# Kernel optimization log

Hardware: AMD Instinct MI355X
Metric: run time of the kernel (lower is better)

Reference implementation:

```python
import jax, jax.numpy as jnp
from jax import lax
import numpy as np

B, T, F_IN, H = 64, 128, 12, 128  # batch, seq_len, input/output features, hidden


def _uinit(key, shape, fan):
    return jax.random.uniform(key, shape, jnp.float32, -1.0, 1.0) / np.float32(np.sqrt(fan))


def setup_inputs() -> dict:
    key = jax.random.key(0)
    ks = jax.random.split(key, 12)
    inp = {
        "x": jax.random.normal(ks[0], (B, T, F_IN), jnp.float32),
        # encoder LSTM (gate order i,f,g,o; b = b_ih + b_hh folded together)
        "enc_Wih": _uinit(ks[1], (4 * H, F_IN), H),
        "enc_Whh": _uinit(ks[2], (4 * H, H), H),
        "enc_b": _uinit(ks[3], (4 * H,), H),
        # decoder LSTM (input is the 12-dim teacher-forced x slice)
        "dec_Wih": _uinit(ks[4], (4 * H, F_IN), H),
        "dec_Whh": _uinit(ks[5], (4 * H, H), H),
        "dec_b": _uinit(ks[6], (4 * H,), H),
        # attention: Linear(2H -> H) with bias, then v: Linear(H -> 1, no bias)
        "attn_W": _uinit(ks[7], (H, 2 * H), 2 * H),
        "attn_b": _uinit(ks[8], (H,), 2 * H),
        "v_w": _uinit(ks[9], (H,), H),
        # output layer: Linear(2H -> F_IN)  (intended width; see notes)
        "out_W": _uinit(ks[10], (F_IN, 2 * H), 2 * H),
        "out_b": _uinit(ks[11], (F_IN,), 2 * H),
    }
    return inp


def _lstm_cell(xt, h, c, Wih, Whh, b):
    z = xt @ Wih.T + h @ Whh.T + b  # [B, 4H]
    i, f, g, o = jnp.split(z, 4, axis=-1)
    c = jax.nn.sigmoid(f) * c + jax.nn.sigmoid(i) * jnp.tanh(g)
    h = jax.nn.sigmoid(o) * jnp.tanh(c)
    return h, c


def reference(x, enc_Wih, enc_Whh, enc_b, dec_Wih, dec_Whh, dec_b,
              attn_W, attn_b, v_w, out_W, out_b):
    b_, t_, _ = x.shape
    hdim = enc_Whh.shape[1]
    xs = jnp.swapaxes(x, 0, 1)  # [T, B, F]
    h0 = jnp.zeros((b_, hdim), x.dtype)
    c0 = jnp.zeros((b_, hdim), x.dtype)

    def enc_step(carry, xt):
        h, c = carry
        h, c = _lstm_cell(xt, h, c, enc_Wih, enc_Whh, enc_b)
        return (h, c), h

    (hT, cT), enc_hs = lax.scan(enc_step, (h0, c0), xs)
    enc_out = jnp.swapaxes(enc_hs, 0, 1)  # [B, T, H]

    # split attn weight: cat(hidden, enc_out) @ W.T == hidden@W1.T + enc_out@W2.T
    W1, W2 = attn_W[:, :hdim], attn_W[:, hdim:]
    enc_proj = jnp.einsum("bth,gh->btg", enc_out, W2)  # precompute encoder side

    def dec_step(carry, xt):
        h, c = carry
        h, c = _lstm_cell(xt, h, c, dec_Wih, dec_Whh, dec_b)
        energy = jnp.tanh((h @ W1.T)[:, None, :] + enc_proj + attn_b)  # [B,T,H]
        score = jnp.einsum("bth,h->bt", energy, v_w)
        w = jax.nn.softmax(score, axis=1)  # attention over encoder time
        ctx = jnp.einsum("bt,bth->bh", w, enc_out)
        return (h, c), jnp.concatenate([h, ctx], axis=-1)  # [B, 2H]

    _, dec_ys = lax.scan(dec_step, (hT, cT), xs)
    dec_out = jnp.swapaxes(dec_ys, 0, 1)  # [B, T, 2H]
    return dec_out @ out_W.T + out_b  # [B, T, F]
```

## Files before the change

### kernel.cpp

```cpp
#include <hip/hip_runtime.h>
#include <hip/hip_bf16.h>

#define BB 64
#define TT 128
#define FIN 12
#define HH 128

#define LOG2E 1.4426950408889634f
#define TWO_LOG2E 2.8853900817779268f

typedef float f2v __attribute__((ext_vector_type(2)));
union F4 { float4 v; f2v h[2]; };

__device__ __forceinline__ float fexp2(float x) { return __builtin_amdgcn_exp2f(x); }
__device__ __forceinline__ float frcp(float x)  { return __builtin_amdgcn_rcpf(x); }

__device__ __forceinline__ float tanh_f(float x) {
  return 1.0f - 2.0f * frcp(1.0f + fexp2(TWO_LOG2E * x));
}
__device__ __forceinline__ float sigm_f(float x) {
  return frcp(1.0f + fexp2(-LOG2E * x));
}

template <int CTRL>
__device__ __forceinline__ float dpp_addstage(float v) {
  int s = __builtin_amdgcn_update_dpp(0, __float_as_int(v), CTRL, 0xF, 0xF, true);
  return v + __int_as_float(s);
}
__device__ __forceinline__ float red8(float v) {
  v = dpp_addstage<0xB1>(v);
  v = dpp_addstage<0x4E>(v);
  v = dpp_addstage<0x141>(v);
  return v;
}

#define PKFMA(acc, hh, ww) \
  asm("v_pk_fma_f32 %0, %1, %2, %0" : "+v"(acc) : "v"(hh), "v"(ww))

#define FMA4S(acc, s, v) do { \
  acc.x = fmaf((s), (v).x, acc.x); \
  acc.y = fmaf((s), (v).y, acc.y); \
  acc.z = fmaf((s), (v).z, acc.z); \
  acc.w = fmaf((s), (v).w, acc.w); } while (0)

#define ACC4(hv, wv, a) do { \
  a = fmaf((hv).x, (wv).x, a); a = fmaf((hv).y, (wv).y, a); \
  a = fmaf((hv).z, (wv).z, a); a = fmaf((hv).w, (wv).w, a); } while (0)

__device__ __forceinline__ void lstm_phase(
    const float* __restrict__ Wih, const float* __restrict__ Whh,
    const float* __restrict__ bias, float* __restrict__ Hout ,
    float* __restrict__ xs, float (*hbuf)[160], float* __restrict__ hist,
    const int tid, const int q, const int i, float& c)
{
  const int xo   = (q < 4) ? 3 * q : 0;
  const float xz = (q < 4) ? 1.0f : 0.0f;

  F4 wg[4][4];
  #pragma unroll
  for (int g = 0; g < 4; ++g)
    #pragma unroll
    for (int j = 0; j < 4; ++j)
      wg[g][j].v = *(const float4*)(Whh + ((g * HH + i) * HH) + 16 * q + 4 * j);

  float wx[4][3];
  #pragma unroll
  for (int g = 0; g < 4; ++g)
    #pragma unroll
    for (int j = 0; j < 3; ++j)
      wx[g][j] = Wih[(g * HH + i) * FIN + xo + j] * xz;

  const float bi = bias[i], bf = bias[HH + i], bg = bias[2 * HH + i], bo = bias[3 * HH + i];

  int ts = 0;
  #pragma unroll 1
  for (int half = 0; half < 2; ++half) {
    #pragma unroll 1
    for (int tt = 0; tt < 64; ++tt, ++ts) {
      const int t = half * 64 + tt;
      __syncthreads();
      const float* hb = (const float*)hbuf[ts & 1] + q * 20;
      F4 H[4];
      H[0].v = *(const float4*)(hb + 0);
      H[1].v = *(const float4*)(hb + 4);
      H[2].v = *(const float4*)(hb + 8);
      H[3].v = *(const float4*)(hb + 12);

      const float* xt = xs + t * FIN + xo;
      float x0 = xt[0], x1 = xt[1], x2 = xt[2];
      float ai = wx[0][0] * x0 + wx[0][1] * x1 + wx[0][2] * x2;
      float af = wx[1][0] * x0 + wx[1][1] * x1 + wx[1][2] * x2;
      float ag = wx[2][0] * x0 + wx[2][1] * x1 + wx[2][2] * x2;
      float ao = wx[3][0] * x0 + wx[3][1] * x1 + wx[3][2] * x2;

      f2v A0 = {0.f, 0.f}, A1 = {0.f, 0.f}, A2 = {0.f, 0.f}, A3 = {0.f, 0.f};
      #pragma unroll
      for (int j = 0; j < 4; ++j) {
        PKFMA(A0, H[j].h[0], wg[0][j].h[0]); PKFMA(A0, H[j].h[1], wg[0][j].h[1]);
        PKFMA(A1, H[j].h[0], wg[1][j].h[0]); PKFMA(A1, H[j].h[1], wg[1][j].h[1]);
        PKFMA(A2, H[j].h[0], wg[2][j].h[0]); PKFMA(A2, H[j].h[1], wg[2][j].h[1]);
        PKFMA(A3, H[j].h[0], wg[3][j].h[0]); PKFMA(A3, H[j].h[1], wg[3][j].h[1]);
      }
      ai += A0.x + A0.y; af += A1.x + A1.y;
      ag += A2.x + A2.y; ao += A3.x + A3.y;

      ai = red8(ai); af = red8(af); ag = red8(ag); ao = red8(ao);

      if (q == 0) {
        float zi = sigm_f(ai + bi);
        float zf = sigm_f(af + bf);
        float zg = tanh_f(ag + bg);
        float zo = sigm_f(ao + bo);
        c = fmaf(zf, c, zi * zg);
        float hn = zo * tanh_f(c);
        hbuf[(ts + 1) & 1][(i >> 4) * 20 + (i & 15)] = hn;
        hist[tt * HH + i] = hn;
      }
    }
    __syncthreads();
    {
      float4* dst = (float4*)(Hout + (size_t)(half * 64) * HH);
      const float4* src = (const float4*)hist;
      dst[tid]        = src[tid];
      dst[tid + 1024] = src[tid + 1024];
    }
  }
}

__global__ __launch_bounds__(1024, 4) void lstm_enc_kernel(
    const float* __restrict__ x,
    const float* __restrict__ eWih, const float* __restrict__ eWhh, const float* __restrict__ eb,
    float* __restrict__ encH, float* __restrict__ decH)
{
  const int b   = blockIdx.x;
  const int tid = threadIdx.x;
  const int q   = tid & 7;
  const int i   = tid >> 3;

  __shared__ __align__(16) float xs[TT * FIN];
  __shared__ __align__(16) float hbuf[2][160];
  __shared__ __align__(16) float hist[64 * HH];

  if (tid < (TT * FIN / 4))
    ((float4*)xs)[tid] = ((const float4*)(x + (size_t)b * TT * FIN))[tid];
  if (tid < 320) ((float*)hbuf)[tid] = 0.0f;
  float c = 0.0f;

  lstm_phase(eWih, eWhh, eb, encH + (size_t)b * TT * HH, xs, hbuf, hist, tid, q, i, c);

  if (q == 0) decH[(size_t)b * TT * HH + i] = c;
}

__global__ __launch_bounds__(1024, 4) void lstm_dec_p_kernel(
    const float* __restrict__ x,
    const float* __restrict__ dWih, const float* __restrict__ dWhh, const float* __restrict__ db,
    const float* __restrict__ attnW,
    const float* __restrict__ encH,
    float* __restrict__ decH, float* __restrict__ Pbuf)
{
  __shared__ __align__(16) float smem[12416];
  const int tid = threadIdx.x;

  if (blockIdx.x < 64) {
    const int b = blockIdx.x;
    const int q = tid & 7;
    const int i = tid >> 3;
    float* xs           = smem;
    float (*hbuf)[160]  = (float(*)[160])(smem + 1536);
    float* hist         = smem + 1856;

    if (tid < (TT * FIN / 4))
      ((float4*)xs)[tid] = ((const float4*)(x + (size_t)b * TT * FIN))[tid];
    if (tid < 128) {
      float hv = encH[((size_t)b * TT + 127) * HH + tid];
      hbuf[0][(tid >> 4) * 20 + (tid & 15)] = hv;
    }
    float c = 0.0f;
    if (q == 0) c = decH[(size_t)b * TT * HH + i];

    lstm_phase(dWih, dWhh, db, decH + (size_t)b * TT * HH, xs, hbuf, hist, tid, q, i, c);
  } else {
    const int pb = blockIdx.x - 64;
    const int b  = pb & 63;
    const int r0 = (pb >> 6) * 64;
    float* WT = smem;
    float* Xt = smem + 4224;

    const float* X = encH + ((size_t)b * TT + r0) * HH;
    ((float4*)Xt)[tid]        = ((const float4*)X)[tid];
    ((float4*)Xt)[tid + 1024] = ((const float4*)X)[tid + 1024];

    const float* W = attnW + HH;
    const int hq = tid & 31, rr = tid >> 5;
    const int h0 = 4 * hq;

    float4 acc0 = make_float4(0.f, 0.f, 0.f, 0.f);
    float4 acc1 = acc0;

    #pragma unroll 1
    for (int kb = 0; kb < 4; ++kb) {
      __syncthreads();
      {
        int h = tid >> 3, koff = (tid & 7) * 4;
        float4 v = *(const float4*)(W + h * 256 + kb * 32 + koff);
        WT[(koff + 0) * 132 + h] = v.x;
        WT[(koff + 1) * 132 + h] = v.y;
        WT[(koff + 2) * 132 + h] = v.z;
        WT[(koff + 3) * 132 + h] = v.w;
      }
      __syncthreads();
      const float* xr0 = Xt + (2 * rr) * 128 + kb * 32;
      const float* xr1 = xr0 + 128;
      #pragma unroll
      for (int k4 = 0; k4 < 32; k4 += 4) {
        float4 xa = *(const float4*)(xr0 + k4);
        float4 xb = *(const float4*)(xr1 + k4);
        float4 w0 = *(const float4*)&WT[(k4 + 0) * 132 + h0];
        float4 w1 = *(const float4*)&WT[(k4 + 1) * 132 + h0];
        float4 w2 = *(const float4*)&WT[(k4 + 2) * 132 + h0];
        float4 w3 = *(const float4*)&WT[(k4 + 3) * 132 + h0];
        FMA4S(acc0, xa.x, w0); FMA4S(acc0, xa.y, w1);
        FMA4S(acc0, xa.z, w2); FMA4S(acc0, xa.w, w3);
        FMA4S(acc1, xb.x, w0); FMA4S(acc1, xb.y, w1);
        FMA4S(acc1, xb.z, w2); FMA4S(acc1, xb.w, w3);
      }
    }
    acc0.x = fexp2(TWO_LOG2E * acc0.x); acc0.y = fexp2(TWO_LOG2E * acc0.y);
    acc0.z = fexp2(TWO_LOG2E * acc0.z); acc0.w = fexp2(TWO_LOG2E * acc0.w);
    acc1.x = fexp2(TWO_LOG2E * acc1.x); acc1.y = fexp2(TWO_LOG2E * acc1.y);
    acc1.z = fexp2(TWO_LOG2E * acc1.z); acc1.w = fexp2(TWO_LOG2E * acc1.w);
    float* O = Pbuf + ((size_t)b * TT + r0) * HH;
    *(float4*)(O + (2 * rr) * 128 + h0)     = acc0;
    *(float4*)(O + (2 * rr + 1) * 128 + h0) = acc1;
  }
}

__global__ __launch_bounds__(256, 2) void projA_kernel(
    const float* __restrict__ decH, const float* __restrict__ attnW,
    const float* __restrict__ attnb, float* __restrict__ Abuf)
{
  const int b  = blockIdx.x & 63;
  const int r0 = (blockIdx.x >> 6) * 16;
  const int tid = threadIdx.x;

  __shared__ __align__(16) float WT[64 * 128];
  __shared__ __align__(16) float Xt[16 * 128];

  const float* X = decH + ((size_t)b * TT + r0) * HH;
  const float* W = attnW;

  ((float4*)Xt)[tid]       = ((const float4*)X)[tid];
  ((float4*)Xt)[256 + tid] = ((const float4*)X)[256 + tid];

  const int hq = tid & 31, rr = tid >> 5;
  const int h0 = 4 * hq;

  float4 acc0 = *(const float4*)(attnb + h0);
  float4 acc1 = acc0;

  for (int kb = 0; kb < 2; ++kb) {
    __syncthreads();
    {
      int h = tid >> 1, koff = (tid & 1) * 32;
      #pragma unroll
      for (int j = 0; j < 8; ++j) {
        float4 v = *(const float4*)(W + h * 256 + kb * 64 + koff + 4 * j);
        int kp = koff + 4 * j;
        WT[(kp + 0) * 128 + h] = v.x;
        WT[(kp + 1) * 128 + h] = v.y;
        WT[(kp + 2) * 128 + h] = v.z;
        WT[(kp + 3) * 128 + h] = v.w;
      }
    }
    __syncthreads();
    const float* xr0 = Xt + (2 * rr) * 128 + kb * 64;
    const float* xr1 = xr0 + 128;
    #pragma unroll
    for (int k4 = 0; k4 < 64; k4 += 4) {
      float4 xa = *(const float4*)(xr0 + k4);
      float4 xb = *(const float4*)(xr1 + k4);
      float4 w0 = *(const float4*)&WT[(k4 + 0) * 128 + h0];
      float4 w1 = *(const float4*)&WT[(k4 + 1) * 128 + h0];
      float4 w2 = *(const float4*)&WT[(k4 + 2) * 128 + h0];
      float4 w3 = *(const float4*)&WT[(k4 + 3) * 128 + h0];
      FMA4S(acc0, xa.x, w0); FMA4S(acc0, xa.y, w1);
      FMA4S(acc0, xa.z, w2); FMA4S(acc0, xa.w, w3);
      FMA4S(acc1, xb.x, w0); FMA4S(acc1, xb.y, w1);
      FMA4S(acc1, xb.z, w2); FMA4S(acc1, xb.w, w3);
    }
  }
  acc0.x = fexp2(TWO_LOG2E * acc0.x); acc0.y = fexp2(TWO_LOG2E * acc0.y);
  acc0.z = fexp2(TWO_LOG2E * acc0.z); acc0.w = fexp2(TWO_LOG2E * acc0.w);
  acc1.x = fexp2(TWO_LOG2E * acc1.x); acc1.y = fexp2(TWO_LOG2E * acc1.y);
  acc1.z = fexp2(TWO_LOG2E * acc1.z); acc1.w = fexp2(TWO_LOG2E * acc1.w);
  float* O = Abuf + ((size_t)b * TT + r0) * HH;
  *(float4*)(O + (2 * rr) * 128 + h0)     = acc0;
  *(float4*)(O + (2 * rr + 1) * 128 + h0) = acc1;
}

#define AST 132

__global__ __launch_bounds__(512, 2) void attn_kernel(
    const float* __restrict__ encH, const float* __restrict__ decH,
    const float* __restrict__ Pbuf, const float* __restrict__ Abuf,
    const float* __restrict__ vw, const float* __restrict__ outW,
    const float* __restrict__ outb, float* __restrict__ out)
{
  const int b  = blockIdx.x >> 3;
  const int s0 = (blockIdx.x & 7) * 16;
  const int tid = threadIdx.x;

  __shared__ __align__(16) float buf[64 * 128];
  __shared__ __align__(16) float a_lds[16 * AST];
  __shared__ __align__(16) float sc[16 * AST];
  __shared__ __align__(16) float dh[16 * 128];
  __shared__ __align__(16) float vl[HH];

  ((float4*)dh)[tid] = ((const float4*)(decH + ((size_t)b * TT + s0) * HH))[tid];
  if (tid < 32) ((float4*)vl)[tid] = ((const float4*)vw)[tid];
  {
    int r = tid >> 5, c4 = (tid & 31) * 4;
    float4 av = *(const float4*)(Abuf + ((size_t)b * TT + s0 + r) * HH + c4);
    *(float4*)&a_lds[r * AST + c4] = av;
  }

  const int u  = tid & 31;
  const int sl = tid >> 5;
  const int uq = u & 15;
  const int uh = u >> 4;

  for (int half = 0; half < 2; ++half) {
    const int tbase = half * 64;
    __syncthreads();
    #pragma unroll
    for (int i = 0; i < 4; ++i) {
      int flat = i * 2048 + tid * 4;
      int tp = flat >> 7;
      int h0 = flat & 127;
      float4 v = *(const float4*)(Pbuf + ((size_t)b * TT + tbase + tp) * HH + h0);
      int tq = tp >> 2, tr = tp & 3;
      buf[(h0 + 0) * 64 + 4 * ((tq ^ ((h0 + 0) >> 2)) & 15) + tr] = v.x;
      buf[(h0 + 1) * 64 + 4 * ((tq ^ ((h0 + 1) >> 2)) & 15) + tr] = v.y;
      buf[(h0 + 2) * 64 + 4 * ((tq ^ ((h0 + 2) >> 2)) & 15) + tr] = v.z;
      buf[(h0 + 3) * 64 + 4 * ((tq ^ ((h0 + 3) >> 2)) & 15) + tr] = v.w;
    }
    __syncthreads();
    float4 acc = make_float4(0.f, 0.f, 0.f, 0.f);
    const float* earow = a_lds + sl * AST;
    #pragma unroll 4
    for (int hh = 0; hh < 64; hh += 4) {
      const int h = uh * 64 + hh;
      float4 ea = *(const float4*)&earow[h];
      float4 va = *(const float4*)&vl[h];
      const int xoff = 4 * ((uq ^ ((h >> 2) & 15)) & 15);
      float4 p0 = *(const float4*)&buf[(h + 0) * 64 + xoff];
      float4 p1 = *(const float4*)&buf[(h + 1) * 64 + xoff];
      float4 p2 = *(const float4*)&buf[(h + 2) * 64 + xoff];
      float4 p3 = *(const float4*)&buf[(h + 3) * 64 + xoff];
      acc.x = fmaf(va.x, frcp(fmaf(ea.x, p0.x, 1.f)), acc.x);
      acc.y = fmaf(va.x, frcp(fmaf(ea.x, p0.y, 1.f)), acc.y);
      acc.z = fmaf(va.x, frcp(fmaf(ea.x, p0.z, 1.f)), acc.z);
      acc.w = fmaf(va.x, frcp(fmaf(ea.x, p0.w, 1.f)), acc.w);
      acc.x = fmaf(va.y, frcp(fmaf(ea.y, p1.x, 1.f)), acc.x);
      acc.y = fmaf(va.y, frcp(fmaf(ea.y, p1.y, 1.f)), acc.y);
      acc.z = fmaf(va.y, frcp(fmaf(ea.y, p1.z, 1.f)), acc.z);
      acc.w = fmaf(va.y, frcp(fmaf(ea.y, p1.w, 1.f)), acc.w);
      acc.x = fmaf(va.z, frcp(fmaf(ea.z, p2.x, 1.f)), acc.x);
      acc.y = fmaf(va.z, frcp(fmaf(ea.z, p2.y, 1.f)), acc.y);
      acc.z = fmaf(va.z, frcp(fmaf(ea.z, p2.z, 1.f)), acc.z);
      acc.w = fmaf(va.z, frcp(fmaf(ea.z, p2.w, 1.f)), acc.w);
      acc.x = fmaf(va.w, frcp(fmaf(ea.w, p3.x, 1.f)), acc.x);
      acc.y = fmaf(va.w, frcp(fmaf(ea.w, p3.y, 1.f)), acc.y);
      acc.z = fmaf(va.w, frcp(fmaf(ea.w, p3.z, 1.f)), acc.z);
      acc.w = fmaf(va.w, frcp(fmaf(ea.w, p3.w, 1.f)), acc.w);
    }
    acc.x += __shfl_xor(acc.x, 16, 64);
    acc.y += __shfl_xor(acc.y, 16, 64);
    acc.z += __shfl_xor(acc.z, 16, 64);
    acc.w += __shfl_xor(acc.w, 16, 64);
    if (uh == 0) {
      float4 o;
      o.x = -2.f * acc.x; o.y = -2.f * acc.y;
      o.z = -2.f * acc.z; o.w = -2.f * acc.w;
      *(float4*)&sc[sl * AST + tbase + 4 * uq] = o;
    }
  }
  __syncthreads();

  {
    float4 sv = *(const float4*)&sc[sl * AST + 4 * u];
    float mx = fmaxf(fmaxf(sv.x, sv.y), fmaxf(sv.z, sv.w));
    #pragma unroll
    for (int msk = 1; msk <= 16; msk <<= 1) mx = fmaxf(mx, __shfl_xor(mx, msk, 64));
    float4 e;
    e.x = fexp2(LOG2E * (sv.x - mx));
    e.y = fexp2(LOG2E * (sv.y - mx));
    e.z = fexp2(LOG2E * (sv.z - mx));
    e.w = fexp2(LOG2E * (sv.w - mx));
    float sm = (e.x + e.y) + (e.z + e.w);
    #pragma unroll
    for (int msk = 1; msk <= 16; msk <<= 1) sm += __shfl_xor(sm, msk, 64);
    float r = frcp(sm);
    e.x *= r; e.y *= r; e.z *= r; e.w *= r;
    *(float4*)&sc[sl * AST + 4 * u] = e;
  }

  float4 ctx = make_float4(0.f, 0.f, 0.f, 0.f);
  const int h0c = 4 * u;
  for (int half = 0; half < 2; ++half) {
    const int tbase = half * 64;
    __syncthreads();
    #pragma unroll
    for (int i = 0; i < 4; ++i) {
      int flat = i * 2048 + tid * 4;
      int tp = flat >> 7;
      int hh0 = flat & 127;
      *(float4*)&buf[tp * 128 + hh0] =
          *(const float4*)(encH + ((size_t)b * TT + tbase + tp) * HH + hh0);
    }
    __syncthreads();
    const float* wrow = sc + sl * AST + tbase;
    #pragma unroll 8
    for (int tp = 0; tp < 64; ++tp) {
      float wt = wrow[tp];
      float4 e4 = *(const float4*)&buf[tp * 128 + h0c];
      FMA4S(ctx, wt, e4);
    }
  }
  __syncthreads();
  *(float4*)&a_lds[sl * AST + h0c] = ctx;
  __syncthreads();

  if (tid < 192) {
    int s = tid / 12, f = tid % 12;
    float acc = outb[f];
    const float4* w4 = (const float4*)(outW + f * 256);
    const float4* d4 = (const float4*)(dh + s * 128);
    const float4* c4 = (const float4*)(a_lds + s * AST);
    #pragma unroll
    for (int k = 0; k < 32; ++k) {
      float4 wv = w4[k], dv = d4[k];
      acc = fmaf(wv.x, dv.x, acc); acc = fmaf(wv.y, dv.y, acc);
      acc = fmaf(wv.z, dv.z, acc); acc = fmaf(wv.w, dv.w, acc);
    }
    #pragma unroll
    for (int k = 0; k < 32; ++k) {
      float4 wv = w4[32 + k], cv = c4[k];
      acc = fmaf(wv.x, cv.x, acc); acc = fmaf(wv.y, cv.y, acc);
      acc = fmaf(wv.z, cv.z, acc); acc = fmaf(wv.w, cv.w, acc);
    }
    out[((size_t)b * TT + s0 + s) * FIN + f] = acc;
  }
}

extern "C" void kernel_launch(void* const* d_in, const int* in_sizes, int n_in,
                              void* d_out, int out_size, void* d_ws, size_t ws_size,
                              hipStream_t stream)
{
  const float* x     = (const float*)d_in[0];
  const float* eWih  = (const float*)d_in[1];
  const float* eWhh  = (const float*)d_in[2];
  const float* eb    = (const float*)d_in[3];
  const float* dWih  = (const float*)d_in[4];
  const float* dWhh  = (const float*)d_in[5];
  const float* db    = (const float*)d_in[6];
  const float* attnW = (const float*)d_in[7];
  const float* attnb = (const float*)d_in[8];
  const float* vw    = (const float*)d_in[9];
  const float* outW  = (const float*)d_in[10];
  const float* outb  = (const float*)d_in[11];
  float* out = (float*)d_out;

  float* ws   = (float*)d_ws;
  const size_t SEG = (size_t)BB * TT * HH;
  float* encH = ws;
  float* decH = ws + SEG;
  float* Pbuf = ws + 2 * SEG;
  float* Abuf = ws + 3 * SEG;

  lstm_enc_kernel<<<64, 1024, 0, stream>>>(x, eWih, eWhh, eb, encH, decH);
  lstm_dec_p_kernel<<<192, 1024, 0, stream>>>(x, dWih, dWhh, db, attnW, encH, decH, Pbuf);
  projA_kernel<<<512, 256, 0, stream>>>(decH, attnW, attnb, Abuf);
  attn_kernel<<<512, 512, 0, stream>>>(encH, decH, Pbuf, Abuf, vw, outW, outb, out);
}
```

Measured before the change: 355.7 us.

## Project encoder states through output weights before attention weighting; drop packed FMA

Measured after the change: 326.4 us. 1.09x faster.

```diff
diff --git a/kernel.cpp b/kernel.cpp
--- a/kernel.cpp
+++ b/kernel.cpp
@@ -8,9 +8,6 @@
 
 #define LOG2E 1.4426950408889634f
 #define TWO_LOG2E 2.8853900817779268f
-
-typedef float f2v __attribute__((ext_vector_type(2)));
-union F4 { float4 v; f2v h[2]; };
 
 __device__ __forceinline__ float fexp2(float x) { return __builtin_amdgcn_exp2f(x); }
 __device__ __forceinline__ float frcp(float x)  { return __builtin_amdgcn_rcpf(x); }
@@ -34,9 +31,6 @@
   return v;
 }
 
-#define PKFMA(acc, hh, ww) \
-  asm("v_pk_fma_f32 %0, %1, %2, %0" : "+v"(acc) : "v"(hh), "v"(ww))
-
 #define FMA4S(acc, s, v) do { \
   acc.x = fmaf((s), (v).x, acc.x); \
   acc.y = fmaf((s), (v).y, acc.y); \
@@ -56,12 +50,12 @@
   const int xo   = (q < 4) ? 3 * q : 0;
   const float xz = (q < 4) ? 1.0f : 0.0f;
 
-  F4 wg[4][4];
+  float4 wg[4][4];
   #pragma unroll
   for (int g = 0; g < 4; ++g)
     #pragma unroll
     for (int j = 0; j < 4; ++j)
-      wg[g][j].v = *(const float4*)(Whh + ((g * HH + i) * HH) + 16 * q + 4 * j);
+      wg[g][j] = *(const float4*)(Whh + ((g * HH + i) * HH) + 16 * q + 4 * j);
 
   float wx[4][3];
   #pragma unroll
@@ -80,11 +74,10 @@
       const int t = half * 64 + tt;
       __syncthreads();
       const float* hb = (const float*)hbuf[ts & 1] + q * 20;
-      F4 H[4];
-      H[0].v = *(const float4*)(hb + 0);
-      H[1].v = *(const float4*)(hb + 4);
-      H[2].v = *(const float4*)(hb + 8);
-      H[3].v = *(const float4*)(hb + 12);
+      float4 h0 = *(const float4*)(hb + 0);
+      float4 h1 = *(const float4*)(hb + 4);
+      float4 h2 = *(const float4*)(hb + 8);
+      float4 h3 = *(const float4*)(hb + 12);
 
       const float* xt = xs + t * FIN + xo;
       float x0 = xt[0], x1 = xt[1], x2 = xt[2];
@@ -93,16 +86,10 @@
       float ag = wx[2][0] * x0 + wx[2][1] * x1 + wx[2][2] * x2;
       float ao = wx[3][0] * x0 + wx[3][1] * x1 + wx[3][2] * x2;
 
-      f2v A0 = {0.f, 0.f}, A1 = {0.f, 0.f}, A2 = {0.f, 0.f}, A3 = {0.f, 0.f};
-      #pragma unroll
-      for (int j = 0; j < 4; ++j) {
-        PKFMA(A0, H[j].h[0], wg[0][j].h[0]); PKFMA(A0, H[j].h[1], wg[0][j].h[1]);
-        PKFMA(A1, H[j].h[0], wg[1][j].h[0]); PKFMA(A1, H[j].h[1], wg[1][j].h[1]);
-        PKFMA(A2, H[j].h[0], wg[2][j].h[0]); PKFMA(A2, H[j].h[1], wg[2][j].h[1]);
-        PKFMA(A3, H[j].h[0], wg[3][j].h[0]); PKFMA(A3, H[j].h[1], wg[3][j].h[1]);
-      }
-      ai += A0.x + A0.y; af += A1.x + A1.y;
-      ag += A2.x + A2.y; ao += A3.x + A3.y;
+      ACC4(h0, wg[0][0], ai); ACC4(h0, wg[1][0], af); ACC4(h0, wg[2][0], ag); ACC4(h0, wg[3][0], ao);
+      ACC4(h1, wg[0][1], ai); ACC4(h1, wg[1][1], af); ACC4(h1, wg[2][1], ag); ACC4(h1, wg[3][1], ao);
+      ACC4(h2, wg[0][2], ai); ACC4(h2, wg[1][2], af); ACC4(h2, wg[2][2], ag); ACC4(h2, wg[3][2], ao);
+      ACC4(h3, wg[0][3], ai); ACC4(h3, wg[1][3], af); ACC4(h3, wg[2][3], ag); ACC4(h3, wg[3][3], ao);
 
       ai = red8(ai); af = red8(af); ag = red8(ag); ao = red8(ao);
 
@@ -299,6 +286,7 @@
 }
 
 #define AST 132
+#define Y2ST 20
 
 __global__ __launch_bounds__(512, 2) void attn_kernel(
     const float* __restrict__ encH, const float* __restrict__ decH,
@@ -315,6 +303,8 @@
   __shared__ __align__(16) float sc[16 * AST];
   __shared__ __align__(16) float dh[16 * 128];
   __shared__ __align__(16) float vl[HH];
+  __shared__ __align__(16) float y2s[TT * Y2ST];
+  __shared__ __align__(16) float w2l[12 * AST];
 
   ((float4*)dh)[tid] = ((const float4*)(decH + ((size_t)b * TT + s0) * HH))[tid];
   if (tid < 32) ((float4*)vl)[tid] = ((const float4*)vw)[tid];
@@ -322,6 +312,11 @@
     int r = tid >> 5, c4 = (tid & 31) * 4;
     float4 av = *(const float4*)(Abuf + ((size_t)b * TT + s0 + r) * HH + c4);
     *(float4*)&a_lds[r * AST + c4] = av;
+  }
+  if (tid < 384) {
+    int f = tid >> 5, k = (tid & 31) * 4;
+    float4 wv = *(const float4*)(outW + f * 256 + 128 + k);
+    *(float4*)&w2l[f * AST + k] = wv;
   }
 
   const int u  = tid & 31;
@@ -405,8 +400,6 @@
     *(float4*)&sc[sl * AST + 4 * u] = e;
   }
 
-  float4 ctx = make_float4(0.f, 0.f, 0.f, 0.f);
-  const int h0c = 4 * u;
   for (int half = 0; half < 2; ++half) {
     const int tbase = half * 64;
     __syncthreads();
@@ -419,36 +412,52 @@
           *(const float4*)(encH + ((size_t)b * TT + tbase + tp) * HH + hh0);
     }
     __syncthreads();
-    const float* wrow = sc + sl * AST + tbase;
-    #pragma unroll 8
-    for (int tp = 0; tp < 64; ++tp) {
-      float wt = wrow[tp];
-      float4 e4 = *(const float4*)&buf[tp * 128 + h0c];
-      FMA4S(ctx, wt, e4);
+    {
+      int j = tid;
+      int t = j / 12, f = j - 12 * t;
+      float a = 0.f;
+      const float* br = buf + t * 128;
+      const float* wr = w2l + f * AST;
+      #pragma unroll 8
+      for (int k = 0; k < 32; ++k) {
+        float4 bv = *(const float4*)(br + 4 * k);
+        float4 wv = *(const float4*)(wr + 4 * k);
+        ACC4(bv, wv, a);
+      }
+      y2s[(tbase + t) * Y2ST + f] = a;
+      if (tid < 256) {
+        int j2 = tid + 512;
+        int t2 = j2 / 12, f2 = j2 - 12 * t2;
+        float a2 = 0.f;
+        const float* br2 = buf + t2 * 128;
+        const float* wr2 = w2l + f2 * AST;
+        #pragma unroll 8
+        for (int k = 0; k < 32; ++k) {
+          float4 bv = *(const float4*)(br2 + 4 * k);
+          float4 wv = *(const float4*)(wr2 + 4 * k);
+          ACC4(bv, wv, a2);
+        }
+        y2s[(tbase + t2) * Y2ST + f2] = a2;
+      }
     }
   }
   __syncthreads();
-  *(float4*)&a_lds[sl * AST + h0c] = ctx;
-  __syncthreads();
 
   if (tid < 192) {
-    int s = tid / 12, f = tid % 12;
+    int s = tid / 12, f = tid - 12 * (tid / 12);
     float acc = outb[f];
     const float4* w4 = (const float4*)(outW + f * 256);
     const float4* d4 = (const float4*)(dh + s * 128);
-    const float4* c4 = (const float4*)(a_lds + s * AST);
     #pragma unroll
     for (int k = 0; k < 32; ++k) {
       float4 wv = w4[k], dv = d4[k];
       acc = fmaf(wv.x, dv.x, acc); acc = fmaf(wv.y, dv.y, acc);
       acc = fmaf(wv.z, dv.z, acc); acc = fmaf(wv.w, dv.w, acc);
     }
-    #pragma unroll
-    for (int k = 0; k < 32; ++k) {
-      float4 wv = w4[32 + k], cv = c4[k];
-      acc = fmaf(wv.x, cv.x, acc); acc = fmaf(wv.y, cv.y, acc);
-      acc = fmaf(wv.z, cv.z, acc); acc = fmaf(wv.w, cv.w, acc);
-    }
+    const float* wrow = sc + s * AST;
+    #pragma unroll 8
+    for (int t = 0; t < TT; ++t)
+      acc = fmaf(wrow[t], y2s[t * Y2ST + f], acc);
     out[((size_t)b * TT + s0 + s) * FIN + f] = acc;
   }
 }
```
